# Kernel optimization log

Hardware: AMD Instinct MI355X
Metric: run time of the kernel (lower is better)

The kernel has to match this reference:

```python
import jax, jax.numpy as jnp
import numpy as np


def setup_inputs() -> dict:
    key = jax.random.key(0)
    x = jax.random.normal(key, (8, 4096, 1024), dtype=jnp.float32)
    return {"x": x}


def reference(x):
    # Causal cumulative mean over time axis: out[b,t] = mean(x[b,:t+1], axis=0)
    B, T, C = x.shape
    csum = jnp.cumsum(x, axis=1)                       # (B, T, C)
    denom = jnp.arange(1, T + 1, dtype=x.dtype)[None, :, None]
    return csum / denom
```

## Files before the change

kernel.cpp:

```cpp
#include <hip/hip_runtime.h>


constexpr int B_SZ   = 8;
constexpr int T_SZ   = 4096;
constexpr int C_SZ   = 1024;
constexpr int CHUNK  = 64;
constexpr int NCHUNK = T_SZ / CHUNK;
constexpr int C4     = C_SZ / 4;

__global__ __launch_bounds__(C4) void cummean_partial(
    const float4* __restrict__ x, float4* __restrict__ part) {
    const int k = blockIdx.x;
    const int b = blockIdx.y;
    const int c = threadIdx.x;

    const float4* xp = x + (size_t)(b * T_SZ + k * CHUNK) * C4 + c;
    float4 s = make_float4(0.f, 0.f, 0.f, 0.f);
#pragma unroll 8
    for (int t = 0; t < CHUNK; ++t) {
        float4 v = xp[(size_t)t * C4];
        s.x += v.x; s.y += v.y; s.z += v.z; s.w += v.w;
    }
    part[(size_t)(b * NCHUNK + k) * C4 + c] = s;
}

__global__ __launch_bounds__(C4) void cummean_scan(
    const float4* __restrict__ x, const float4* __restrict__ part,
    float4* __restrict__ out) {
    const int k = blockIdx.x;
    const int b = blockIdx.y;
    const int c = threadIdx.x;

    float4 run = make_float4(0.f, 0.f, 0.f, 0.f);
    const float4* pp = part + (size_t)b * NCHUNK * C4 + c;
    for (int j = 0; j < k; ++j) {
        float4 v = pp[(size_t)j * C4];
        run.x += v.x; run.y += v.y; run.z += v.z; run.w += v.w;
    }

    const size_t base = (size_t)(b * T_SZ + k * CHUNK) * C4 + c;
    const float4* xp = x + base;
    float4*       op = out + base;
    const int t0 = k * CHUNK;
#pragma unroll 4
    for (int t = 0; t < CHUNK; ++t) {
        float4 v = xp[(size_t)t * C4];
        run.x += v.x; run.y += v.y; run.z += v.z; run.w += v.w;
        const float inv = 1.0f / (float)(t0 + t + 1);
        float4 o;
        o.x = run.x * inv; o.y = run.y * inv; o.z = run.z * inv; o.w = run.w * inv;
        op[(size_t)t * C4] = o;
    }
}

extern "C" void kernel_launch(void* const* d_in, const int* in_sizes, int n_in,
                              void* d_out, int out_size, void* d_ws, size_t ws_size,
                              hipStream_t stream) {
    const float4* x   = (const float4*)d_in[0];
    float4*       out = (float4*)d_out;
    float4*       part = (float4*)d_ws;

    dim3 grid(NCHUNK, B_SZ);
    cummean_partial<<<grid, C4, 0, stream>>>(x, part);
    cummean_scan<<<grid, C4, 0, stream>>>(x, part, out);
}
```

Measured before the change: 264.7 us.

## Add exclusive scan kernel over chunk partials and halve chunk size

```diff
diff --git a/kernel.cpp b/kernel.cpp
--- a/kernel.cpp
+++ b/kernel.cpp
@@ -4,49 +4,55 @@
 constexpr int B_SZ   = 8;
 constexpr int T_SZ   = 4096;
 constexpr int C_SZ   = 1024;
-constexpr int CHUNK  = 64;
+constexpr int CHUNK  = 32;
 constexpr int NCHUNK = T_SZ / CHUNK;
 constexpr int C4     = C_SZ / 4;
 
 __global__ __launch_bounds__(C4) void cummean_partial(
     const float4* __restrict__ x, float4* __restrict__ part) {
-    const int k = blockIdx.x;
-    const int b = blockIdx.y;
-    const int c = threadIdx.x;
+    const int k = blockIdx.x, b = blockIdx.y, c = threadIdx.x;
+    const float4* xp = x + (size_t)(b * T_SZ + k * CHUNK) * C4 + c;
+    float s0x=0.f,s0y=0.f,s0z=0.f,s0w=0.f, s1x=0.f,s1y=0.f,s1z=0.f,s1w=0.f;
+#pragma unroll 8
+    for (int t = 0; t < CHUNK; t += 2) {
+        float4 a = xp[(size_t)t * C4];
+        float4 d = xp[(size_t)(t + 1) * C4];
+        s0x += a.x; s0y += a.y; s0z += a.z; s0w += a.w;
+        s1x += d.x; s1y += d.y; s1z += d.z; s1w += d.w;
+    }
+    float4 s; s.x = s0x + s1x; s.y = s0y + s1y; s.z = s0z + s1z; s.w = s0w + s1w;
+    part[(size_t)(b * NCHUNK + k) * C4 + c] = s;
+}
 
-    const float4* xp = x + (size_t)(b * T_SZ + k * CHUNK) * C4 + c;
-    float4 s = make_float4(0.f, 0.f, 0.f, 0.f);
-#pragma unroll 8
-    for (int t = 0; t < CHUNK; ++t) {
-        float4 v = xp[(size_t)t * C4];
-        s.x += v.x; s.y += v.y; s.z += v.z; s.w += v.w;
+__global__ __launch_bounds__(C4) void cummean_scanpart(float4* __restrict__ part) {
+    const int b = blockIdx.x, c = threadIdx.x;
+    float4* pp = part + (size_t)b * NCHUNK * C4 + c;
+    float rx=0.f, ry=0.f, rz=0.f, rw=0.f;
+#pragma unroll 4
+    for (int k = 0; k < NCHUNK; ++k) {
+        float4 v = pp[(size_t)k * C4];
+        float4 e; e.x = rx; e.y = ry; e.z = rz; e.w = rw;
+        pp[(size_t)k * C4] = e;
+        rx += v.x; ry += v.y; rz += v.z; rw += v.w;
     }
-    part[(size_t)(b * NCHUNK + k) * C4 + c] = s;
 }
 
 __global__ __launch_bounds__(C4) void cummean_scan(
     const float4* __restrict__ x, const float4* __restrict__ part,
     float4* __restrict__ out) {
-    const int k = blockIdx.x;
-    const int b = blockIdx.y;
-    const int c = threadIdx.x;
+    const int k = blockIdx.x, b = blockIdx.y, c = threadIdx.x;
 
-    float4 run = make_float4(0.f, 0.f, 0.f, 0.f);
-    const float4* pp = part + (size_t)b * NCHUNK * C4 + c;
-    for (int j = 0; j < k; ++j) {
-        float4 v = pp[(size_t)j * C4];
-        run.x += v.x; run.y += v.y; run.z += v.z; run.w += v.w;
-    }
+    float4 run = part[(size_t)(b * NCHUNK + k) * C4 + c];
 
     const size_t base = (size_t)(b * T_SZ + k * CHUNK) * C4 + c;
     const float4* xp = x + base;
     float4*       op = out + base;
     const int t0 = k * CHUNK;
-#pragma unroll 4
+#pragma unroll 8
     for (int t = 0; t < CHUNK; ++t) {
         float4 v = xp[(size_t)t * C4];
         run.x += v.x; run.y += v.y; run.z += v.z; run.w += v.w;
-        const float inv = 1.0f / (float)(t0 + t + 1);
+        const float inv = __builtin_amdgcn_rcpf((float)(t0 + t + 1));
         float4 o;
         o.x = run.x * inv; o.y = run.y * inv; o.z = run.z * inv; o.w = run.w * inv;
         op[(size_t)t * C4] = o;
@@ -56,11 +62,12 @@
 extern "C" void kernel_launch(void* const* d_in, const int* in_sizes, int n_in,
                               void* d_out, int out_size, void* d_ws, size_t ws_size,
                               hipStream_t stream) {
-    const float4* x   = (const float4*)d_in[0];
-    float4*       out = (float4*)d_out;
+    const float4* x    = (const float4*)d_in[0];
+    float4*       out  = (float4*)d_out;
     float4*       part = (float4*)d_ws;
 
     dim3 grid(NCHUNK, B_SZ);
     cummean_partial<<<grid, C4, 0, stream>>>(x, part);
+    cummean_scanpart<<<B_SZ, C4, 0, stream>>>(part);
     cummean_scan<<<grid, C4, 0, stream>>>(x, part, out);
 }
```

New measurement: 266.5 us. Within noise of the previous version (+0.7%).
